# Kernel optimization log

Measured on AMD Instinct MI355X. Metric: run time of the kernel, lower is better.

## Reference

```python
import jax, jax.numpy as jnp
import numpy as np

B, S, D, H = 4, 2048, 1024, 16
HD = D // H

def setup_inputs() -> dict:
    key = jax.random.key(0)
    ks = jax.random.split(key, 9)
    sc = 0.02
    return {
        "x": jax.random.normal(ks[0], (B, S, D), dtype=jnp.float32),
        "Wq": jax.random.normal(ks[1], (D, D), dtype=jnp.float32) * sc,
        "bq": jax.random.normal(ks[2], (D,), dtype=jnp.float32) * sc,
        "Wk": jax.random.normal(ks[3], (D, D), dtype=jnp.float32) * sc,
        "bk": jax.random.normal(ks[4], (D,), dtype=jnp.float32) * sc,
        "Wv": jax.random.normal(ks[5], (D, D), dtype=jnp.float32) * sc,
        "bv": jax.random.normal(ks[6], (D,), dtype=jnp.float32) * sc,
        "Wo": jax.random.normal(ks[7], (D, D), dtype=jnp.float32) * sc,
        "bo": jax.random.normal(ks[8], (D,), dtype=jnp.float32) * sc,
    }

def reference(x, Wq, bq, Wk, bk, Wv, bv, Wo, bo):
    b, n, d = x.shape
    # projections, split heads: [b, h, n, hd]
    def split_heads(t):
        return t.reshape(b, n, H, HD).transpose(0, 2, 1, 3)
    q = split_heads(x @ Wq.T + bq)
    k = split_heads(x @ Wk.T + bk)
    v = split_heads(x @ Wv.T + bv)
    # scores [b, h, n, n], causal mask (triu above diagonal -> -inf)
    scores = jnp.einsum("bhqd,bhkd->bhqk", q, k)
    causal = jnp.tril(jnp.ones((n, n), dtype=bool))  # True = keep
    scores = jnp.where(causal, scores, -jnp.inf)
    # note: module divides by sqrt(head_dim) AFTER masking, same result
    attn = jax.nn.softmax(scores / jnp.sqrt(jnp.float32(HD)), axis=-1)
    ctx = jnp.einsum("bhqk,bhkd->bhqd", attn, v)
    ctx = ctx.transpose(0, 2, 1, 3).reshape(b, n, d)
    return ctx @ Wo.T + bo
```

## Files before the change

kernel.cpp:

```cpp
#include <hip/hip_runtime.h>
#include <stdint.h>

#define BATCH 4
#define S_LEN 2048
#define D_DIM 1024
#define NH 16
#define HD 64
#define M_ROWS (BATCH * S_LEN)
#define NQB (S_LEN / 128)

using u16 = unsigned short;
typedef __attribute__((ext_vector_type(8))) __bf16 bf16x8;
typedef __attribute__((ext_vector_type(4))) float f32x4;
typedef __attribute__((ext_vector_type(16))) float f32x16;
typedef __attribute__((ext_vector_type(8))) unsigned short u16x8;

__device__ __forceinline__ u16 f2bf(float f) {
  unsigned u = __builtin_bit_cast(unsigned, f);
  u += 0x7fffu + ((u >> 16) & 1u);
  return (u16)(u >> 16);
}
__device__ __forceinline__ unsigned pk2(float lo, float hi) {
  return (unsigned)f2bf(lo) | ((unsigned)f2bf(hi) << 16);
}

__global__ void cvt_bf16_kernel(const float* __restrict__ in, u16* __restrict__ out, int n4) {
  int i = blockIdx.x * blockDim.x + threadIdx.x;
  if (i < n4) {
    float4 v = ((const float4*)in)[i];
    ushort4 o;
    o.x = f2bf(v.x); o.y = f2bf(v.y); o.z = f2bf(v.z); o.w = f2bf(v.w);
    ((ushort4*)out)[i] = o;
  }
}

template<int MODE>
__global__ __launch_bounds__(256)
void gemm_bt_kernel(const u16* __restrict__ A, const u16* __restrict__ Bt,
                    const float* __restrict__ bias, void* __restrict__ Cout,
                    int M, int N, int K, float scale) {
  __shared__ __align__(16) u16 As[128 * 64];
  __shared__ __align__(16) u16 Bs[128 * 64];
  const int tid = threadIdx.x;
  const int w = tid >> 6;
  const int lane = tid & 63;
  const int l15 = lane & 15, l4 = lane >> 4;
  const int m0 = blockIdx.y * 128, n0 = blockIdx.x * 128;
  const int wr = (w >> 1) * 64, wc = (w & 1) * 64;

  f32x4 acc[4][4] = {};

  for (int k0 = 0; k0 < K; k0 += 64) {
    __syncthreads();
#pragma unroll
    for (int i = 0; i < 4; ++i) {
      int chunk = w * 4 + i;
      int o = chunk * 1024 + lane * 16;
      int row = o >> 7;
      int g = (o >> 4) & 7;
      int gs = g ^ (row & 7);
      const u16* gA = A + (size_t)(m0 + row) * K + k0 + gs * 8;
      const u16* gB = Bt + (size_t)(n0 + row) * K + k0 + gs * 8;
      __builtin_amdgcn_global_load_lds((const __attribute__((address_space(1))) void*)gA,
                                       (__attribute__((address_space(3))) void*)(As + chunk * 512),
                                       16, 0, 0);
      __builtin_amdgcn_global_load_lds((const __attribute__((address_space(1))) void*)gB,
                                       (__attribute__((address_space(3))) void*)(Bs + chunk * 512),
                                       16, 0, 0);
    }
    __syncthreads();

    bf16x8 a[4][2];
#pragma unroll
    for (int mb = 0; mb < 4; ++mb) {
#pragma unroll
      for (int ks = 0; ks < 2; ++ks) {
        int row = wr + mb * 16 + l15;
        int gsw = (ks * 4 + l4) ^ (row & 7);
        a[mb][ks] = *(const bf16x8*)(As + row * 64 + gsw * 8);
      }
    }
#pragma unroll
    for (int nb = 0; nb < 4; ++nb) {
      int row = wc + nb * 16 + l15;
      int g0 = (0 + l4) ^ (row & 7);
      int g1 = (4 + l4) ^ (row & 7);
      bf16x8 b0 = *(const bf16x8*)(Bs + row * 64 + g0 * 8);
      bf16x8 b1 = *(const bf16x8*)(Bs + row * 64 + g1 * 8);
#pragma unroll
      for (int mb = 0; mb < 4; ++mb) {
        acc[mb][nb] = __builtin_amdgcn_mfma_f32_16x16x32_bf16(a[mb][0], b0, acc[mb][nb], 0, 0, 0);
        acc[mb][nb] = __builtin_amdgcn_mfma_f32_16x16x32_bf16(a[mb][1], b1, acc[mb][nb], 0, 0, 0);
      }
    }
  }

#pragma unroll
  for (int mb = 0; mb < 4; ++mb) {
#pragma unroll
    for (int nb = 0; nb < 4; ++nb) {
#pragma unroll
      for (int r = 0; r < 4; ++r) {
        int m = m0 + wr + mb * 16 + l4 * 4 + r;
        int n = n0 + wc + nb * 16 + l15;
        float v = (acc[mb][nb][r] + bias[n]) * scale;
        if (MODE == 0) {
          int bb = m >> 11;
          int ss = m & (S_LEN - 1);
          int hh = n >> 6;
          int hd = n & (HD - 1);
          ((u16*)Cout)[(((size_t)bb * NH + hh) * S_LEN + ss) * HD + hd] = f2bf(v);
        } else {
          ((float*)Cout)[(size_t)m * N + n] = v;
        }
      }
    }
  }
}

__device__ __forceinline__ void stage_k(const u16* __restrict__ Kg, size_t base, int kt,
                                        u16* Kd, int w, int lane) {
#pragma unroll
  for (int i = 0; i < 2; ++i) {
    int ic = w * 2 + i;
    int c = ic * 64 + lane;
    int row = c >> 3, g = c & 7, gs = g ^ (row & 7);
    __builtin_amdgcn_global_load_lds(
        (const __attribute__((address_space(1))) void*)(Kg + base + (size_t)(kt * 64 + row) * HD + gs * 8),
        (__attribute__((address_space(3))) void*)(Kd + ic * 512), 16, 0, 0);
  }
}

__device__ __forceinline__ void pfrag(const f32x16& st, int hi, bf16x8& fa, bf16x8& fb) {
  unsigned c0 = pk2(st[0], st[1]),   c1 = pk2(st[2], st[3]);
  unsigned c2 = pk2(st[4], st[5]),   c3 = pk2(st[6], st[7]);
  unsigned c4 = pk2(st[8], st[9]),   c5 = pk2(st[10], st[11]);
  unsigned c6 = pk2(st[12], st[13]), c7 = pk2(st[14], st[15]);
  unsigned p0 = __shfl_xor(c0, 32), p1 = __shfl_xor(c1, 32);
  unsigned p2 = __shfl_xor(c2, 32), p3 = __shfl_xor(c3, 32);
  unsigned p4 = __shfl_xor(c4, 32), p5 = __shfl_xor(c5, 32);
  unsigned p6 = __shfl_xor(c6, 32), p7 = __shfl_xor(c7, 32);
  union { unsigned u[4]; bf16x8 v; } a, b;
  a.u[0] = hi ? p2 : c0; a.u[1] = hi ? p3 : c1;
  a.u[2] = hi ? c2 : p0; a.u[3] = hi ? c3 : p1;
  b.u[0] = hi ? p6 : c4; b.u[1] = hi ? p7 : c5;
  b.u[2] = hi ? c6 : p4; b.u[3] = hi ? c7 : p5;
  fa = a.v; fb = b.v;
}

__global__ __launch_bounds__(256)
void attn_kernel(const u16* __restrict__ Q, const u16* __restrict__ Kg,
                 const u16* __restrict__ Vg, u16* __restrict__ ctx) {
  __shared__ __align__(16) u16 Ks[2][64 * 64];
  __shared__ __align__(16) u16 Vt[64 * 64];

  const int tid = threadIdx.x;
  const int w = tid >> 6, lane = tid & 63;
  const int l31 = lane & 31, hi = lane >> 5;
  const int hi4 = hi * 4, hi8 = hi * 8;
  const int bh = blockIdx.y;
  const size_t base = (size_t)bh * S_LEN * HD;
  const int b = bh >> 4, h = bh & (NH - 1);

  const int vrow = tid >> 2;
  const int vc0 = (tid & 3) * 16;

#pragma unroll 1
  for (int seg = 0; seg < 2; ++seg) {
    const int qb = seg ? (NQB - 1 - blockIdx.x) : blockIdx.x;
    const int Qw = qb * 128 + w * 32;
    const int q_g = Qw + l31;

    bf16x8 qf[4];
#pragma unroll
    for (int step = 0; step < 4; ++step)
      qf[step] = *(const bf16x8*)(Q + base + (size_t)q_g * HD + step * 16 + hi8);

    f32x16 oacc0 = {}, oacc1 = {};
    float mrun = -1e30f, lrun = 0.f;

    const int nkt = 2 * qb + 2;

    stage_k(Kg, base, 0, Ks[0], w, lane);
    u16x8 vv0, vv1;
    {
      const u16* gv = Vg + base + (size_t)vrow * HD + vc0;
      vv0 = *(const u16x8*)gv;
      vv1 = *(const u16x8*)(gv + 8);
    }

    for (int kt = 0; kt < nkt; ++kt) {
      const int cur = kt & 1;
      const bool more = (kt + 1 < nkt);

#pragma unroll
      for (int j = 0; j < 8; ++j) {
        int d0 = vc0 + j;
        Vt[d0 * 64 + (((vrow >> 3) ^ ((d0 >> 2) & 7)) << 3) + (vrow & 7)] = vv0[j];
        int d1 = vc0 + 8 + j;
        Vt[d1 * 64 + (((vrow >> 3) ^ ((d1 >> 2) & 7)) << 3) + (vrow & 7)] = vv1[j];
      }
      __syncthreads();

      if (more) {
        stage_k(Kg, base, kt + 1, Ks[cur ^ 1], w, lane);
        const u16* gv = Vg + base + (size_t)((kt + 1) * 64 + vrow) * HD + vc0;
        vv0 = *(const u16x8*)gv;
        vv1 = *(const u16x8*)(gv + 8);
      }

      const u16* Kb = &Ks[cur][0];

      if (kt * 64 <= Qw + 31) {
        f32x16 st0 = {}, st1 = {};
#pragma unroll
        for (int step = 0; step < 4; ++step) {
          int r0 = l31, r1 = 32 + l31;
          bf16x8 kf0 = *(const bf16x8*)(Kb + r0 * 64 + (((step * 2 + hi) ^ (r0 & 7)) << 3));
          bf16x8 kf1 = *(const bf16x8*)(Kb + r1 * 64 + (((step * 2 + hi) ^ (r1 & 7)) << 3));
          st0 = __builtin_amdgcn_mfma_f32_32x32x16_bf16(kf0, qf[step], st0, 0, 0, 0);
          st1 = __builtin_amdgcn_mfma_f32_32x32x16_bf16(kf1, qf[step], st1, 0, 0, 0);
        }

        if (kt * 64 + 63 > Qw) {
#pragma unroll
          for (int r = 0; r < 16; ++r) {
            int key0 = kt * 64 + hi4 + (r & 3) + 8 * (r >> 2);
            if (key0 > q_g) st0[r] = -1e30f;
            if (key0 + 32 > q_g) st1[r] = -1e30f;
          }
        }

        float tm = -1e30f;
#pragma unroll
        for (int r = 0; r < 16; ++r) { tm = fmaxf(tm, st0[r]); tm = fmaxf(tm, st1[r]); }
        tm = fmaxf(tm, __shfl_xor(tm, 32));

        if (__any(tm > mrun)) {
          float mnew = fmaxf(mrun, tm);
          float rs = __expf(mrun - mnew);
          mrun = mnew;
          lrun *= rs;
#pragma unroll
          for (int r = 0; r < 16; ++r) {
            float rsb = __shfl(rs, (r & 3) + 8 * (r >> 2) + hi4);
            oacc0[r] *= rsb;
            oacc1[r] *= rsb;
          }
        }

        float sum = 0.f;
#pragma unroll
        for (int r = 0; r < 16; ++r) {
          st0[r] = __expf(st0[r] - mrun); sum += st0[r];
          st1[r] = __expf(st1[r] - mrun); sum += st1[r];
        }
        sum += __shfl_xor(sum, 32);
        lrun += sum;

        bf16x8 paf0, paf1, paf2, paf3;
        pfrag(st0, hi, paf0, paf1);
        pfrag(st1, hi, paf2, paf3);

#pragma unroll
        for (int ks = 0; ks < 4; ++ks) {
          bf16x8 pa = (ks == 0) ? paf0 : (ks == 1) ? paf1 : (ks == 2) ? paf2 : paf3;
          int d0 = l31;
          bf16x8 vf0 = *(const bf16x8*)(Vt + d0 * 64 + (((ks * 2 + hi) ^ ((d0 >> 2) & 7)) << 3));
          int d1 = 32 + l31;
          bf16x8 vf1 = *(const bf16x8*)(Vt + d1 * 64 + (((ks * 2 + hi) ^ ((d1 >> 2) & 7)) << 3));
          oacc0 = __builtin_amdgcn_mfma_f32_32x32x16_bf16(pa, vf0, oacc0, 0, 0, 0);
          oacc1 = __builtin_amdgcn_mfma_f32_32x32x16_bf16(pa, vf1, oacc1, 0, 0, 0);
        }
      }
      __syncthreads();
    }

#pragma unroll
    for (int r = 0; r < 16; ++r) {
      float lr = __shfl(lrun, (r & 3) + 8 * (r >> 2) + hi4);
      float inv = 1.0f / lr;
      int srow = Qw + (r & 3) + 8 * (r >> 2) + hi4;
      size_t rowbase = ((size_t)b * S_LEN + srow) * D_DIM + h * HD;
      ctx[rowbase + l31] = f2bf(oacc0[r] * inv);
      ctx[rowbase + 32 + l31] = f2bf(oacc1[r] * inv);
    }
  }
}

extern "C" void kernel_launch(void* const* d_in, const int* in_sizes, int n_in,
                              void* d_out, int out_size, void* d_ws, size_t ws_size,
                              hipStream_t stream) {
  const float* x  = (const float*)d_in[0];
  const float* Wq = (const float*)d_in[1];
  const float* bq = (const float*)d_in[2];
  const float* Wk = (const float*)d_in[3];
  const float* bk = (const float*)d_in[4];
  const float* Wv = (const float*)d_in[5];
  const float* bv = (const float*)d_in[6];
  const float* Wo = (const float*)d_in[7];
  const float* bo = (const float*)d_in[8];

  char* ws = (char*)d_ws;
  const size_t MB = 1024 * 1024;
  u16* xb   = (u16*)(ws + 0);
  u16* Wqb  = (u16*)(ws + 16 * MB);
  u16* Wkb  = (u16*)(ws + 18 * MB);
  u16* Wvb  = (u16*)(ws + 20 * MB);
  u16* Wob  = (u16*)(ws + 22 * MB);
  u16* Qb   = (u16*)(ws + 24 * MB);
  u16* Kb   = (u16*)(ws + 40 * MB);
  u16* Vb   = (u16*)(ws + 56 * MB);
  u16* ctxb = xb;

  cvt_bf16_kernel<<<(M_ROWS * D_DIM / 4 + 255) / 256, 256, 0, stream>>>(x, xb, M_ROWS * D_DIM / 4);
  cvt_bf16_kernel<<<(D_DIM * D_DIM / 4 + 255) / 256, 256, 0, stream>>>(Wq, Wqb, D_DIM * D_DIM / 4);
  cvt_bf16_kernel<<<(D_DIM * D_DIM / 4 + 255) / 256, 256, 0, stream>>>(Wk, Wkb, D_DIM * D_DIM / 4);
  cvt_bf16_kernel<<<(D_DIM * D_DIM / 4 + 255) / 256, 256, 0, stream>>>(Wv, Wvb, D_DIM * D_DIM / 4);
  cvt_bf16_kernel<<<(D_DIM * D_DIM / 4 + 255) / 256, 256, 0, stream>>>(Wo, Wob, D_DIM * D_DIM / 4);

  dim3 gg(D_DIM / 128, M_ROWS / 128);
  gemm_bt_kernel<0><<<gg, 256, 0, stream>>>(xb, Wqb, bq, Qb, M_ROWS, D_DIM, D_DIM, 0.125f);
  gemm_bt_kernel<0><<<gg, 256, 0, stream>>>(xb, Wkb, bk, Kb, M_ROWS, D_DIM, D_DIM, 1.0f);
  gemm_bt_kernel<0><<<gg, 256, 0, stream>>>(xb, Wvb, bv, Vb, M_ROWS, D_DIM, D_DIM, 1.0f);

  attn_kernel<<<dim3(NQB / 2, BATCH * NH), 256, 0, stream>>>(Qb, Kb, Vb, ctxb);

  gemm_bt_kernel<1><<<gg, 256, 0, stream>>>(ctxb, Wob, bo, (float*)d_out, M_ROWS, D_DIM, D_DIM, 1.0f);
}
```

Baseline: 223.8 us.

## Fuse QKV projections into one GEMM, batch weight casts, use exp2 softmax

Merges the Q, K and V projection GEMMs into a single launch over a concatenated weight matrix, choosing bias, scale and destination per column block. The four weight conversions become one kernel, cutting launch count and giving the fused GEMM a larger grid. Q is pre-scaled by log2(e)/sqrt(hd) so the softmax can use the hardware exp2 instruction instead of __expf. The V transpose-staging thread mapping is also changed, and the output GEMM gets its own specialised kernel.

```diff
diff --git a/kernel.cpp b/kernel.cpp
--- a/kernel.cpp
+++ b/kernel.cpp
@@ -8,12 +8,15 @@
 #define HD 64
 #define M_ROWS (BATCH * S_LEN)
 #define NQB (S_LEN / 128)
+#define QSCALE 0.18033688011f
 
 using u16 = unsigned short;
 typedef __attribute__((ext_vector_type(8))) __bf16 bf16x8;
 typedef __attribute__((ext_vector_type(4))) float f32x4;
 typedef __attribute__((ext_vector_type(16))) float f32x16;
 typedef __attribute__((ext_vector_type(8))) unsigned short u16x8;
+
+__device__ __forceinline__ float exp2fast(float x) { return __builtin_amdgcn_exp2f(x); }
 
 __device__ __forceinline__ u16 f2bf(float f) {
   unsigned u = __builtin_bit_cast(unsigned, f);
@@ -34,11 +37,37 @@
   }
 }
 
-template<int MODE>
+__global__ void cvt_w_kernel(const float* __restrict__ W0, const float* __restrict__ W1,
+                             const float* __restrict__ W2, const float* __restrict__ W3,
+                             u16* __restrict__ out) {
+  int y = blockIdx.y;
+  const float* src = (y == 0) ? W0 : (y == 1) ? W1 : (y == 2) ? W2 : W3;
+  u16* dst = out + (size_t)y * D_DIM * D_DIM;
+  int i = blockIdx.x * blockDim.x + threadIdx.x;
+  float4 v = ((const float4*)src)[i];
+  ushort4 o;
+  o.x = f2bf(v.x); o.y = f2bf(v.y); o.z = f2bf(v.z); o.w = f2bf(v.w);
+  ((ushort4*)dst)[i] = o;
+}
+
+__device__ __forceinline__ void stage_tile(const u16* __restrict__ src, int srcK,
+                                           u16* dst, int w, int lane) {
+#pragma unroll
+  for (int i = 0; i < 4; ++i) {
+    int ic = w * 4 + i;
+    int c = ic * 64 + lane;
+    int row = c >> 3, g = c & 7, gs = g ^ (row & 7);
+    __builtin_amdgcn_global_load_lds(
+        (const __attribute__((address_space(1))) void*)(src + (size_t)row * srcK + gs * 8),
+        (__attribute__((address_space(3))) void*)(dst + ic * 512), 16, 0, 0);
+  }
+}
+
 __global__ __launch_bounds__(256)
-void gemm_bt_kernel(const u16* __restrict__ A, const u16* __restrict__ Bt,
-                    const float* __restrict__ bias, void* __restrict__ Cout,
-                    int M, int N, int K, float scale) {
+void gemm_qkv_kernel(const u16* __restrict__ A, const u16* __restrict__ Bt,
+                     const float* __restrict__ bq, const float* __restrict__ bk,
+                     const float* __restrict__ bv,
+                     u16* __restrict__ Qo, u16* __restrict__ Ko, u16* __restrict__ Vo) {
   __shared__ __align__(16) u16 As[128 * 64];
   __shared__ __align__(16) u16 Bs[128 * 64];
   const int tid = threadIdx.x;
@@ -47,27 +76,14 @@
   const int l15 = lane & 15, l4 = lane >> 4;
   const int m0 = blockIdx.y * 128, n0 = blockIdx.x * 128;
   const int wr = (w >> 1) * 64, wc = (w & 1) * 64;
+  const int K = D_DIM;
 
   f32x4 acc[4][4] = {};
 
   for (int k0 = 0; k0 < K; k0 += 64) {
     __syncthreads();
-#pragma unroll
-    for (int i = 0; i < 4; ++i) {
-      int chunk = w * 4 + i;
-      int o = chunk * 1024 + lane * 16;
-      int row = o >> 7;
-      int g = (o >> 4) & 7;
-      int gs = g ^ (row & 7);
-      const u16* gA = A + (size_t)(m0 + row) * K + k0 + gs * 8;
-      const u16* gB = Bt + (size_t)(n0 + row) * K + k0 + gs * 8;
-      __builtin_amdgcn_global_load_lds((const __attribute__((address_space(1))) void*)gA,
-                                       (__attribute__((address_space(3))) void*)(As + chunk * 512),
-                                       16, 0, 0);
-      __builtin_amdgcn_global_load_lds((const __attribute__((address_space(1))) void*)gB,
-                                       (__attribute__((address_space(3))) void*)(Bs + chunk * 512),
-                                       16, 0, 0);
-    }
+    stage_tile(A + (size_t)m0 * K + k0, K, As, w, lane);
+    stage_tile(Bt + (size_t)n0 * K + k0, K, Bs, w, lane);
     __syncthreads();
 
     bf16x8 a[4][2];
@@ -95,6 +111,11 @@
     }
   }
 
+  const int which = n0 >> 10;
+  const float* bias = (which == 0) ? bq : (which == 1) ? bk : bv;
+  u16* dst = (which == 0) ? Qo : (which == 1) ? Ko : Vo;
+  const float scale = (which == 0) ? QSCALE : 1.0f;
+
 #pragma unroll
   for (int mb = 0; mb < 4; ++mb) {
 #pragma unroll
@@ -103,16 +124,73 @@
       for (int r = 0; r < 4; ++r) {
         int m = m0 + wr + mb * 16 + l4 * 4 + r;
         int n = n0 + wc + nb * 16 + l15;
-        float v = (acc[mb][nb][r] + bias[n]) * scale;
-        if (MODE == 0) {
-          int bb = m >> 11;
-          int ss = m & (S_LEN - 1);
-          int hh = n >> 6;
-          int hd = n & (HD - 1);
-          ((u16*)Cout)[(((size_t)bb * NH + hh) * S_LEN + ss) * HD + hd] = f2bf(v);
-        } else {
-          ((float*)Cout)[(size_t)m * N + n] = v;
-        }
+        int col = n & 1023;
+        float v = (acc[mb][nb][r] + bias[col]) * scale;
+        int bb = m >> 11;
+        int ss = m & (S_LEN - 1);
+        int hh = col >> 6;
+        int hd = col & (HD - 1);
+        dst[(((size_t)bb * NH + hh) * S_LEN + ss) * HD + hd] = f2bf(v);
+      }
+    }
+  }
+}
+
+__global__ __launch_bounds__(256)
+void gemm_out_kernel(const u16* __restrict__ A, const u16* __restrict__ Bt,
+                     const float* __restrict__ bias, float* __restrict__ Cout) {
+  __shared__ __align__(16) u16 As[128 * 64];
+  __shared__ __align__(16) u16 Bs[128 * 64];
+  const int tid = threadIdx.x;
+  const int w = tid >> 6;
+  const int lane = tid & 63;
+  const int l15 = lane & 15, l4 = lane >> 4;
+  const int m0 = blockIdx.y * 128, n0 = blockIdx.x * 128;
+  const int wr = (w >> 1) * 64, wc = (w & 1) * 64;
+  const int K = D_DIM, N = D_DIM;
+
+  f32x4 acc[4][4] = {};
+
+  for (int k0 = 0; k0 < K; k0 += 64) {
+    __syncthreads();
+    stage_tile(A + (size_t)m0 * K + k0, K, As, w, lane);
+    stage_tile(Bt + (size_t)n0 * K + k0, K, Bs, w, lane);
+    __syncthreads();
+
+    bf16x8 a[4][2];
+#pragma unroll
+    for (int mb = 0; mb < 4; ++mb) {
+#pragma unroll
+      for (int ks = 0; ks < 2; ++ks) {
+        int row = wr + mb * 16 + l15;
+        int gsw = (ks * 4 + l4) ^ (row & 7);
+        a[mb][ks] = *(const bf16x8*)(As + row * 64 + gsw * 8);
+      }
+    }
+#pragma unroll
+    for (int nb = 0; nb < 4; ++nb) {
+      int row = wc + nb * 16 + l15;
+      int g0 = (0 + l4) ^ (row & 7);
+      int g1 = (4 + l4) ^ (row & 7);
+      bf16x8 b0 = *(const bf16x8*)(Bs + row * 64 + g0 * 8);
+      bf16x8 b1 = *(const bf16x8*)(Bs + row * 64 + g1 * 8);
+#pragma unroll
+      for (int mb = 0; mb < 4; ++mb) {
+        acc[mb][nb] = __builtin_amdgcn_mfma_f32_16x16x32_bf16(a[mb][0], b0, acc[mb][nb], 0, 0, 0);
+        acc[mb][nb] = __builtin_amdgcn_mfma_f32_16x16x32_bf16(a[mb][1], b1, acc[mb][nb], 0, 0, 0);
+      }
+    }
+  }
+
+#pragma unroll
+  for (int mb = 0; mb < 4; ++mb) {
+#pragma unroll
+    for (int nb = 0; nb < 4; ++nb) {
+#pragma unroll
+      for (int r = 0; r < 4; ++r) {
+        int m = m0 + wr + mb * 16 + l4 * 4 + r;
+        int n = n0 + wc + nb * 16 + l15;
+        Cout[(size_t)m * N + n] = acc[mb][nb][r] + bias[n];
       }
     }
   }
@@ -162,8 +240,8 @@
   const size_t base = (size_t)bh * S_LEN * HD;
   const int b = bh >> 4, h = bh & (NH - 1);
 
-  const int vrow = tid >> 2;
-  const int vc0 = (tid & 3) * 16;
+  const int vkey = tid & 63;
+  const int vd0 = (tid >> 6) * 16;
 
 #pragma unroll 1
   for (int seg = 0; seg < 2; ++seg) {
@@ -184,7 +262,7 @@
     stage_k(Kg, base, 0, Ks[0], w, lane);
     u16x8 vv0, vv1;
     {
-      const u16* gv = Vg + base + (size_t)vrow * HD + vc0;
+      const u16* gv = Vg + base + (size_t)vkey * HD + vd0;
       vv0 = *(const u16x8*)gv;
       vv1 = *(const u16x8*)(gv + 8);
     }
@@ -195,16 +273,16 @@
 
 #pragma unroll
       for (int j = 0; j < 8; ++j) {
-        int d0 = vc0 + j;
-        Vt[d0 * 64 + (((vrow >> 3) ^ ((d0 >> 2) & 7)) << 3) + (vrow & 7)] = vv0[j];
-        int d1 = vc0 + 8 + j;
-        Vt[d1 * 64 + (((vrow >> 3) ^ ((d1 >> 2) & 7)) << 3) + (vrow & 7)] = vv1[j];
+        int d0 = vd0 + j;
+        Vt[d0 * 64 + (((vkey >> 3) ^ ((d0 >> 2) & 7)) << 3) + (vkey & 7)] = vv0[j];
+        int d1 = vd0 + 8 + j;
+        Vt[d1 * 64 + (((vkey >> 3) ^ ((d1 >> 2) & 7)) << 3) + (vkey & 7)] = vv1[j];
       }
       __syncthreads();
 
       if (more) {
         stage_k(Kg, base, kt + 1, Ks[cur ^ 1], w, lane);
-        const u16* gv = Vg + base + (size_t)((kt + 1) * 64 + vrow) * HD + vc0;
+        const u16* gv = Vg + base + (size_t)((kt + 1) * 64 + vkey) * HD + vd0;
         vv0 = *(const u16x8*)gv;
         vv1 = *(const u16x8*)(gv + 8);
       }
@@ -238,7 +316,7 @@
 
         if (__any(tm > mrun)) {
           float mnew = fmaxf(mrun, tm);
-          float rs = __expf(mrun - mnew);
+          float rs = exp2fast(mrun - mnew);
           mrun = mnew;
           lrun *= rs;
 #pragma unroll
@@ -252,8 +330,8 @@
         float sum = 0.f;
 #pragma unroll
         for (int r = 0; r < 16; ++r) {
-          st0[r] = __expf(st0[r] - mrun); sum += st0[r];
-          st1[r] = __expf(st1[r] - mrun); sum += st1[r];
+          st0[r] = exp2fast(st0[r] - mrun); sum += st0[r];
+          st1[r] = exp2fast(st1[r] - mrun); sum += st1[r];
         }
         sum += __shfl_xor(sum, 32);
         lrun += sum;
@@ -303,28 +381,22 @@
 
   char* ws = (char*)d_ws;
   const size_t MB = 1024 * 1024;
-  u16* xb   = (u16*)(ws + 0);
-  u16* Wqb  = (u16*)(ws + 16 * MB);
-  u16* Wkb  = (u16*)(ws + 18 * MB);
-  u16* Wvb  = (u16*)(ws + 20 * MB);
-  u16* Wob  = (u16*)(ws + 22 * MB);
-  u16* Qb   = (u16*)(ws + 24 * MB);
-  u16* Kb   = (u16*)(ws + 40 * MB);
-  u16* Vb   = (u16*)(ws + 56 * MB);
-  u16* ctxb = xb;
+  u16* xb     = (u16*)(ws + 0);
+  u16* Wqkvb  = (u16*)(ws + 16 * MB);
+  u16* Wob    = (u16*)(ws + 22 * MB);
+  u16* Qb     = (u16*)(ws + 24 * MB);
+  u16* Kb     = (u16*)(ws + 40 * MB);
+  u16* Vb     = (u16*)(ws + 56 * MB);
+  u16* ctxb   = xb;
 
   cvt_bf16_kernel<<<(M_ROWS * D_DIM / 4 + 255) / 256, 256, 0, stream>>>(x, xb, M_ROWS * D_DIM / 4);
-  cvt_bf16_kernel<<<(D_DIM * D_DIM / 4 + 255) / 256, 256, 0, stream>>>(Wq, Wqb, D_DIM * D_DIM / 4);
-  cvt_bf16_kernel<<<(D_DIM * D_DIM / 4 + 255) / 256, 256, 0, stream>>>(Wk, Wkb, D_DIM * D_DIM / 4);
-  cvt_bf16_kernel<<<(D_DIM * D_DIM / 4 + 255) / 256, 256, 0, stream>>>(Wv, Wvb, D_DIM * D_DIM / 4);
-  cvt_bf16_kernel<<<(D_DIM * D_DIM / 4 + 255) / 256, 256, 0, stream>>>(Wo, Wob, D_DIM * D_DIM / 4);
-
-  dim3 gg(D_DIM / 128, M_ROWS / 128);
-  gemm_bt_kernel<0><<<gg, 256, 0, stream>>>(xb, Wqb, bq, Qb, M_ROWS, D_DIM, D_DIM, 0.125f);
-  gemm_bt_kernel<0><<<gg, 256, 0, stream>>>(xb, Wkb, bk, Kb, M_ROWS, D_DIM, D_DIM, 1.0f);
-  gemm_bt_kernel<0><<<gg, 256, 0, stream>>>(xb, Wvb, bv, Vb, M_ROWS, D_DIM, D_DIM, 1.0f);
+  cvt_w_kernel<<<dim3(D_DIM * D_DIM / 4 / 256, 4), 256, 0, stream>>>(Wq, Wk, Wv, Wo, Wqkvb);
+
+  gemm_qkv_kernel<<<dim3(3 * D_DIM / 128, M_ROWS / 128), 256, 0, stream>>>(
+      xb, Wqkvb, bq, bk, bv, Qb, Kb, Vb);
 
   attn_kernel<<<dim3(NQB / 2, BATCH * NH), 256, 0, stream>>>(Qb, Kb, Vb, ctxb);
 
-  gemm_bt_kernel<1><<<gg, 256, 0, stream>>>(ctxb, Wob, bo, (float*)d_out, M_ROWS, D_DIM, D_DIM, 1.0f);
-}
+  gemm_out_kernel<<<dim3(D_DIM / 128, M_ROWS / 128), 256, 0, stream>>>(
+      ctxb, Wob, bo, (float*)d_out);
+}
```

New measurement: 200.9 us. 10.2% less time.
